# Performance work log

Hardware: AMD Instinct MI355X
Metric: run time of the kernel (lower is better)

Reference implementation:

```python
import jax, jax.numpy as jnp
import numpy as np

B, S, D, H = 2, 2048, 1024, 16
DH = D // H


def setup_inputs() -> dict:
    key = jax.random.key(0)
    ks = jax.random.split(key, 12)
    f = lambda k, sh: jax.random.normal(k, sh, dtype=jnp.float32)
    inp = {"q": f(ks[0], (B, S, D)), "k": f(ks[1], (B, S, D)), "v": f(ks[2], (B, S, D))}
    scale = 1.0 / np.sqrt(D)
    names = ["q", "k", "v", "o"]
    for i, n in enumerate(names):
        inp["W" + n] = f(ks[3 + i], (D, D)) * scale
        inp["b" + n] = f(ks[7 + i], (D,)) * scale
    # causal mask: True = masked out
    inp["mask"] = jnp.triu(jnp.ones((S, S), dtype=bool), k=1)[None, None]
    return inp


def _rope(x):
    # x: [b, h, s, dh]; non-standard RoPE from AbsPositionEncoding
    s, dh = x.shape[2], x.shape[3]
    inv = jnp.exp(jnp.arange(0, dh, 2, dtype=jnp.float32) * (-(4.0 * jnp.log(jnp.float32(10.0))) / dh))
    pos = jnp.arange(s, dtype=jnp.float32)[:, None]
    sin = jnp.sin(pos * inv)  # [s, dh/2]
    cos = jnp.cos(pos * inv)
    x1 = x[..., 0::2]
    x2 = x[..., 1::2]
    out = jnp.stack([x1 * sin - x2 * cos, -x1 * cos - x2 * sin], axis=-1)
    return out.reshape(x.shape)


def reference(q, k, v, Wq, bq, Wk, bk, Wv, bv, Wo, bo, mask):
    b, s, d = q.shape
    h, dh = H, DH

    def proj(x, W, bias):
        return (x @ W.T + bias).reshape(b, -1, h, dh).transpose(0, 2, 1, 3)

    Q = proj(q, Wq, bq)
    K = proj(k, Wk, bk)
    V = proj(v, Wv, bv)
    PQ = _rope(Q)
    PK = _rope(K)
    # NOTE: source's forward() path applies NO 1/sqrt(dh) scaling
    scores = jnp.einsum('bhqd,bhkd->bhqk', PQ, PK)
    neg = jnp.finfo(scores.dtype).min
    scores = jnp.where(mask, neg, scores)
    p = jax.nn.softmax(scores, axis=-1)
    p = jnp.where(mask, jnp.float32(0.0), p)
    out = jnp.einsum('bhqk,bhkd->bhqd', p, V)
    out = out.transpose(0, 2, 1, 3).reshape(b, s, d)
    return out @ Wo.T + bo
```

## Files before the change

### kernel.cpp

```cpp
#include <hip/hip_runtime.h>
#include <stdint.h>

#define BB 2
#define SS 2048
#define DD 1024
#define HH 16
#define DH 64
#define MM 4096

typedef __attribute__((ext_vector_type(8))) short short8;
typedef __attribute__((ext_vector_type(4))) float floatx4;
typedef __attribute__((ext_vector_type(16))) float floatx16;
typedef unsigned short u16;

#define MFMA16(a,b,c) __builtin_amdgcn_mfma_f32_16x16x32_bf16((a),(b),(c),0,0,0)
#define MFMA32(a,b,c) __builtin_amdgcn_mfma_f32_32x32x16_bf16((a),(b),(c),0,0,0)

__device__ __forceinline__ u16 f2bf(float f) {
  unsigned u = __float_as_uint(f);
  u += 0x7fffu + ((u >> 16) & 1u);
  return (u16)(u >> 16);
}

__device__ __forceinline__ unsigned cvtpk(float lo, float hi2) {
  unsigned r;
  asm("v_cvt_pk_bf16_f32 %0, %1, %2" : "=v"(r) : "v"(lo), "v"(hi2));
  return r;
}

__device__ __forceinline__ void gll16(const void* g, void* l) {
  __builtin_amdgcn_global_load_lds((const __attribute__((address_space(1))) void*)g,
                                   (__attribute__((address_space(3))) void*)l,
                                   16, 0, 0);
}

__global__ __launch_bounds__(256) void prep(
    const float* __restrict__ q, const float* __restrict__ k, const float* __restrict__ v,
    const float* __restrict__ Wq, const float* __restrict__ Wk,
    const float* __restrict__ Wv, const float* __restrict__ Wo,
    u16* __restrict__ qb, u16* __restrict__ kb, u16* __restrict__ vb,
    u16* __restrict__ wqb, u16* __restrict__ wkb, u16* __restrict__ wvb, u16* __restrict__ wob,
    float2* __restrict__ tab) {
  int bid = blockIdx.x;
  if (bid < 256) {
    const int t = bid * 256 + threadIdx.x;
    const int s = t >> 5, j = t & 31;
    const float inv = expf(-(float)j * (0.125f * 2.302585092994046f));
    const float a = (float)s * inv;
    tab[t] = make_float2(sinf(a), cosf(a));
    return;
  }
  bid -= 256;
  const float* src;
  u16* dst;
  int x;
  if (bid < 12288) {
    const int z = bid >> 12;
    x = bid & 4095;
    src = z == 0 ? q : (z == 1 ? k : v);
    dst = z == 0 ? qb : (z == 1 ? kb : vb);
  } else {
    bid -= 12288;
    const int z = bid >> 10;
    x = bid & 1023;
    src = z == 0 ? Wq : (z == 1 ? Wk : (z == 2 ? Wv : Wo));
    dst = z == 0 ? wqb : (z == 1 ? wkb : (z == 2 ? wvb : wob));
  }
  const int i = (x * 256 + threadIdx.x) * 4;
  const float4 xv = *(const float4*)(src + i);
  ushort4 p; p.x = f2bf(xv.x); p.y = f2bf(xv.y); p.z = f2bf(xv.z); p.w = f2bf(xv.w);
  *(ushort4*)(dst + i) = p;
}

__device__ __forceinline__ void gemm_core128(const u16* __restrict__ A, const u16* __restrict__ Bt,
                                             int K, u16* As, u16* Bs, floatx4 acc[4][4],
                                             int m0, int n0) {
  const int tid = threadIdx.x;
  const int w = tid >> 6, l = tid & 63;
  const int lr = l & 15, lq = l >> 4;
  const int wm = (w >> 1) * 64, wn = (w & 1) * 64;

#pragma unroll
  for (int i = 0; i < 4; ++i)
#pragma unroll
    for (int j = 0; j < 4; ++j) acc[i][j] = (floatx4){0.f, 0.f, 0.f, 0.f};

  const int srow = w * 32 + (l >> 2);
  const int scol = (l & 3) * 8;
  const u16* ag = A + (size_t)(m0 + srow) * K + scol;
  const u16* bg = Bt + (size_t)(n0 + srow) * K + scol;
  u16* as0 = &As[w * 1024];
  u16* bs0 = &Bs[w * 1024];

  for (int k0 = 0; k0 < K; k0 += 32) {
    gll16(ag + k0, as0);
    gll16(ag + (size_t)16 * K + k0, as0 + 512);
    gll16(bg + k0, bs0);
    gll16(bg + (size_t)16 * K + k0, bs0 + 512);
    __syncthreads();
    short8 af[4], bfv[4];
#pragma unroll
    for (int i = 0; i < 4; ++i) af[i] = *(const short8*)&As[(wm + i * 16 + lr) * 32 + lq * 8];
#pragma unroll
    for (int j = 0; j < 4; ++j) bfv[j] = *(const short8*)&Bs[(wn + j * 16 + lr) * 32 + lq * 8];
    __builtin_amdgcn_s_setprio(1);
#pragma unroll
    for (int i = 0; i < 4; ++i)
#pragma unroll
      for (int j = 0; j < 4; ++j) acc[i][j] = MFMA16(af[i], bfv[j], acc[i][j]);
    __builtin_amdgcn_s_setprio(0);
    __syncthreads();
  }
}

__device__ __forceinline__ void gemm_core64(const u16* __restrict__ A, const u16* __restrict__ Bt,
                                            int K, u16* As, u16* Bs, floatx4 acc[2][4],
                                            int m0, int n0) {
  const int tid = threadIdx.x;
  const int w = tid >> 6, l = tid & 63;
  const int lr = l & 15, lq = l >> 4;
  const int wm = (w >> 1) * 32, wn = (w & 1) * 64;

#pragma unroll
  for (int i = 0; i < 2; ++i)
#pragma unroll
    for (int j = 0; j < 4; ++j) acc[i][j] = (floatx4){0.f, 0.f, 0.f, 0.f};

  const int arow = w * 16 + (l >> 2);
  const int brow = w * 32 + (l >> 2);
  const int scol = (l & 3) * 8;
  const u16* ag = A + (size_t)(m0 + arow) * K + scol;
  const u16* bg = Bt + (size_t)(n0 + brow) * K + scol;
  u16* as0 = &As[w * 512];
  u16* bs0 = &Bs[w * 1024];

  for (int k0 = 0; k0 < K; k0 += 32) {
    gll16(ag + k0, as0);
    gll16(bg + k0, bs0);
    gll16(bg + (size_t)16 * K + k0, bs0 + 512);
    __syncthreads();
    short8 af[2], bfv[4];
#pragma unroll
    for (int i = 0; i < 2; ++i) af[i] = *(const short8*)&As[(wm + i * 16 + lr) * 32 + lq * 8];
#pragma unroll
    for (int j = 0; j < 4; ++j) bfv[j] = *(const short8*)&Bs[(wn + j * 16 + lr) * 32 + lq * 8];
    __builtin_amdgcn_s_setprio(1);
#pragma unroll
    for (int i = 0; i < 2; ++i)
#pragma unroll
      for (int j = 0; j < 4; ++j) acc[i][j] = MFMA16(af[i], bfv[j], acc[i][j]);
    __builtin_amdgcn_s_setprio(0);
    __syncthreads();
  }
}

__global__ __launch_bounds__(256) void gemm3_fused(
    const u16* __restrict__ A0, const u16* __restrict__ A1, const u16* __restrict__ A2,
    const u16* __restrict__ B0, const u16* __restrict__ B1, const u16* __restrict__ B2,
    const float* __restrict__ c0, const float* __restrict__ c1, const float* __restrict__ c2,
    u16* __restrict__ Qro, u16* __restrict__ Kro, u16* __restrict__ Vtr,
    const float2* __restrict__ tab) {
  __shared__ alignas(16) u16 As[128 * 32];
  __shared__ alignas(16) u16 Bs[128 * 32];
  const int z = blockIdx.z;
  const u16* A = z == 0 ? A0 : (z == 1 ? A1 : A2);
  const u16* Bt = z == 0 ? B0 : (z == 1 ? B1 : B2);
  const float* bias = z == 0 ? c0 : (z == 1 ? c1 : c2);
  const int m0 = blockIdx.y * 128, n0 = blockIdx.x * 128;

  floatx4 acc[4][4];
  gemm_core128(A, Bt, DD, As, Bs, acc, m0, n0);

  const int tid = threadIdx.x;
  const int w = tid >> 6, l = tid & 63;
  const int lr = l & 15, lq = l >> 4;
  const int wm = (w >> 1) * 64, wn = (w & 1) * 64;

  if (z == 2) {
#pragma unroll
    for (int i = 0; i < 4; ++i) {
      const int row = m0 + wm + i * 16 + lq * 4;
      const int b = row >> 11, s = row & (SS - 1);
#pragma unroll
      for (int j = 0; j < 4; ++j) {
        const int col = n0 + wn + j * 16 + lr;
        const int h = col >> 6, e = col & 63;
        const float bv = bias[col];
        ushort4 pk;
        pk.x = f2bf(acc[i][j][0] + bv);
        pk.y = f2bf(acc[i][j][1] + bv);
        pk.z = f2bf(acc[i][j][2] + bv);
        pk.w = f2bf(acc[i][j][3] + bv);
        *(ushort4*)(Vtr + ((size_t)(b * HH + h) * DH + e) * SS + s) = pk;
      }
    }
  } else {
    u16* dst = z ? Kro : Qro;
#pragma unroll
    for (int i = 0; i < 4; ++i) {
#pragma unroll
      for (int j = 0; j < 4; ++j) {
        const int col = n0 + wn + j * 16 + lr;
        const int h = col >> 6, e = col & 63;
        const float bv = bias[col];
#pragma unroll
        for (int r = 0; r < 4; ++r) {
          const int row = m0 + wm + i * 16 + lq * 4 + r;
          const int b = row >> 11, s = row & (SS - 1);
          const float v = acc[i][j][r] + bv;
          const float p = __shfl_xor(v, 1);
          const float2 sc = tab[s * 32 + (e >> 1)];
          const float ov = ((e & 1) == 0) ? (v * sc.x - p * sc.y)
                                          : (-p * sc.y - v * sc.x);
          dst[((size_t)(b * HH + h) * SS + s) * DH + e] = f2bf(ov);
        }
      }
    }
  }
}

__global__ __launch_bounds__(256) void gemm_bt(const u16* __restrict__ A, const u16* __restrict__ Bt,
                                               const float* __restrict__ bias, float* __restrict__ C,
                                               int M, int N, int K) {
  __shared__ alignas(16) u16 As[64 * 32];
  __shared__ alignas(16) u16 Bs[128 * 32];
  const int m0 = blockIdx.y * 64, n0 = blockIdx.x * 128;
  floatx4 acc[2][4];
  gemm_core64(A, Bt, K, As, Bs, acc, m0, n0);

  const int tid = threadIdx.x;
  const int w = tid >> 6, l = tid & 63;
  const int lr = l & 15, lq = l >> 4;
  const int wm = (w >> 1) * 32, wn = (w & 1) * 64;
#pragma unroll
  for (int i = 0; i < 2; ++i) {
    const int row = m0 + wm + i * 16 + lq * 4;
#pragma unroll
    for (int j = 0; j < 4; ++j) {
      const int col = n0 + wn + j * 16 + lr;
      const float bv = bias[col];
      float* cp = C + (size_t)row * N + col;
#pragma unroll
      for (int r = 0; r < 4; ++r) cp[(size_t)r * N] = acc[i][j][r] + bv;
    }
  }
}

__global__ __launch_bounds__(64) void attn_fwd(const u16* __restrict__ Qr, const u16* __restrict__ Kr,
                                               const u16* __restrict__ Vt, u16* __restrict__ O) {
  const int bid = blockIdx.x;
  const int qi = 63 - (bid >> 5);
  const int bh = bid & 31;
  const int l = threadIdx.x;
  const int ql = l & 31, hi = l >> 5;
  const int qw0 = qi * 32;
  const u16* Qh = Qr + (size_t)bh * SS * DH;
  const u16* Kh = Kr + (size_t)bh * SS * DH;
  const u16* Vh = Vt + (size_t)bh * DH * SS;

  short8 qf[4];
#pragma unroll
  for (int i = 0; i < 4; ++i)
    qf[i] = *(const short8*)(Qh + (size_t)(qw0 + ql) * DH + i * 16 + hi * 8);

  floatx16 oacc[2];
#pragma unroll
  for (int dt = 0; dt < 2; ++dt)
#pragma unroll
    for (int r = 0; r < 16; ++r) oacc[dt][r] = 0.f;
  float mrun = -1e30f, lrun = 0.f;

  const u16* kbase = Kh + (size_t)ql * DH + hi * 8;
  const u16* vbase = Vh + (size_t)ql * SS + hi * 8;

#define LOADK(kd, kv0)                                                      \
  do {                                                                      \
    const u16* kp_ = kbase + (size_t)(kv0) * DH;                            \
    kd[0] = *(const short8*)(kp_);                                          \
    kd[1] = *(const short8*)(kp_ + 16);                                     \
    kd[2] = *(const short8*)(kp_ + 32);                                     \
    kd[3] = *(const short8*)(kp_ + 48);                                     \
  } while (0)

#define COMPUTE(kd, tt)                                                              \
  do {                                                                               \
    const int kv0_ = (tt) * 32;                                                      \
    floatx16 st;                                                                     \
    _Pragma("unroll") for (int r = 0; r < 16; ++r) st[r] = 0.f;                      \
    __builtin_amdgcn_s_setprio(1);                                                   \
    _Pragma("unroll") for (int i = 0; i < 4; ++i) st = MFMA32(kd[i], qf[i], st);     \
    __builtin_amdgcn_s_setprio(0);                                                   \
    short8 vf[4];                                                                    \
    {                                                                                \
      const u16* vp_ = vbase + kv0_;                                                 \
      vf[0] = *(const short8*)(vp_);                                                 \
      vf[1] = *(const short8*)(vp_ + 16);                                            \
      vf[2] = *(const short8*)(vp_ + (size_t)32 * SS);                               \
      vf[3] = *(const short8*)(vp_ + (size_t)32 * SS + 16);                          \
    }                                                                                \
    if ((tt) == T - 1) {                             \
      _Pragma("unroll") for (int r = 0; r < 16; ++r) {                               \
        const int kv = (r & 3) + 8 * (r >> 2) + 4 * hi;                              \
        if (kv > ql) st[r] = -1e30f;                                                 \
      }                                                                              \
    }                                                                                \
    float m8[8];                                                                     \
    _Pragma("unroll") for (int r = 0; r < 8; ++r) m8[r] = fmaxf(st[r], st[r + 8]);   \
    float m4a = fmaxf(m8[0], m8[4]), m4b = fmaxf(m8[1], m8[5]);                      \
    float m4c = fmaxf(m8[2], m8[6]), m4d = fmaxf(m8[3], m8[7]);                      \
    float tmax = fmaxf(fmaxf(m4a, m4b), fmaxf(m4c, m4d));                            \
    tmax = fmaxf(tmax, __shfl_xor(tmax, 32));                                        \
    const float mn = fmaxf(mrun, tmax);                                              \
    const float sc = __expf(mrun - mn);                                              \
    mrun = mn;                                                                       \
    float ps = 0.f;                                                                  \
    _Pragma("unroll") for (int r = 0; r < 16; ++r) {                                 \
      const float p = __expf(st[r] - mn);                                            \
      st[r] = p;                                                                     \
      ps += p;                                                                       \
    }                                                                                \
    ps += __shfl_xor(ps, 32);                                                        \
    lrun = lrun * sc + ps;                                                           \
    _Pragma("unroll") for (int dt = 0; dt < 2; ++dt)                                 \
      _Pragma("unroll") for (int r = 0; r < 16; ++r) oacc[dt][r] *= sc;              \
    short8 pfrag[2];                                                                 \
    _Pragma("unroll") for (int c = 0; c < 2; ++c) {                                  \
      const int A0r = 2 * c, A1r = A0r + 1;                                          \
      const unsigned P00 = cvtpk(st[4 * A0r + 0], st[4 * A0r + 1]);                  \
      const unsigned P01 = cvtpk(st[4 * A0r + 2], st[4 * A0r + 3]);                  \
      const unsigned P10 = cvtpk(st[4 * A1r + 0], st[4 * A1r + 1]);                  \
      const unsigned P11 = cvtpk(st[4 * A1r + 2], st[4 * A1r + 3]);                  \
      const unsigned S0 = hi ? P00 : P10;                                            \
      const unsigned S1 = hi ? P01 : P11;                                            \
      const unsigned R0 = (unsigned)__shfl_xor((int)S0, 32);                         \
      const unsigned R1 = (unsigned)__shfl_xor((int)S1, 32);                         \
      union { unsigned u[4]; short8 s; } fd;                                         \
      fd.u[0] = hi ? R0 : P00;                                                       \
      fd.u[1] = hi ? R1 : P01;                                                       \
      fd.u[2] = hi ? P10 : R0;                                                       \
      fd.u[3] = hi ? P11 : R1;                                                       \
      pfrag[c] = fd.s;                                                               \
    }                                                                                \
    __builtin_amdgcn_s_setprio(1);                                                   \
    _Pragma("unroll") for (int dt = 0; dt < 2; ++dt)                                 \
      _Pragma("unroll") for (int c = 0; c < 2; ++c)                                  \
        oacc[dt] = MFMA32(vf[dt * 2 + c], pfrag[c], oacc[dt]);                       \
    __builtin_amdgcn_s_setprio(0);                                                   \
  } while (0)

  const int T = qi + 1;
  short8 kA[4], kB[4];
  LOADK(kA, 0);
  int t = 0;
  while (true) {
    if (t + 1 < T) LOADK(kB, (t + 1) * 32);
    COMPUTE(kA, t);
    ++t;
    if (t >= T) break;
    if (t + 1 < T) LOADK(kA, (t + 1) * 32);
    COMPUTE(kB, t);
    ++t;
    if (t >= T) break;
  }
#undef COMPUTE
#undef LOADK

  const float inv = 1.0f / lrun;
  const int b = bh >> 4, h = bh & 15;
  u16* orow = O + ((size_t)(b * SS + qw0 + ql)) * DD + h * DH;
#pragma unroll
  for (int dt = 0; dt < 2; ++dt)
#pragma unroll
    for (int g = 0; g < 4; ++g) {
      ushort4 pk;
      pk.x = f2bf(oacc[dt][4 * g + 0] * inv);
      pk.y = f2bf(oacc[dt][4 * g + 1] * inv);
      pk.z = f2bf(oacc[dt][4 * g + 2] * inv);
      pk.w = f2bf(oacc[dt][4 * g + 3] * inv);
      *(ushort4*)(orow + dt * 32 + 8 * g + 4 * hi) = pk;
    }
}

extern "C" void kernel_launch(void* const* d_in, const int* in_sizes, int n_in,
                              void* d_out, int out_size, void* d_ws, size_t ws_size,
                              hipStream_t stream) {
  (void)in_sizes; (void)n_in; (void)out_size; (void)ws_size;
  const float* q  = (const float*)d_in[0];
  const float* k  = (const float*)d_in[1];
  const float* v  = (const float*)d_in[2];
  const float* Wq = (const float*)d_in[3];
  const float* bq = (const float*)d_in[4];
  const float* Wk = (const float*)d_in[5];
  const float* bk = (const float*)d_in[6];
  const float* Wv = (const float*)d_in[7];
  const float* bv = (const float*)d_in[8];
  const float* Wo = (const float*)d_in[9];
  const float* bo = (const float*)d_in[10];
  float* out = (float*)d_out;

  char* ws = (char*)d_ws;
  size_t off = 0;
  auto carve = [&](size_t bytes) { char* p = ws + off; off += (bytes + 255) & ~(size_t)255; return p; };
  u16* qb   = (u16*)carve((size_t)MM * DD * 2);
  u16* kb   = (u16*)carve((size_t)MM * DD * 2);
  u16* vb   = (u16*)carve((size_t)MM * DD * 2);
  u16* wqb  = (u16*)carve((size_t)DD * DD * 2);
  u16* wkb  = (u16*)carve((size_t)DD * DD * 2);
  u16* wvb  = (u16*)carve((size_t)DD * DD * 2);
  u16* wob  = (u16*)carve((size_t)DD * DD * 2);
  u16* Qro  = (u16*)carve((size_t)MM * DD * 2);
  u16* Kro  = (u16*)carve((size_t)MM * DD * 2);
  u16* Vtr  = (u16*)carve((size_t)MM * DD * 2);
  float2* tab = (float2*)carve((size_t)SS * 32 * 8);
  u16* Ob = qb;

  prep<<<256 + 3 * 4096 + 4 * 1024, 256, 0, stream>>>(q, k, v, Wq, Wk, Wv, Wo,
                                                      qb, kb, vb, wqb, wkb, wvb, wob, tab);
  gemm3_fused<<<dim3(DD / 128, MM / 128, 3), 256, 0, stream>>>(qb, kb, vb, wqb, wkb, wvb,
                                                               bq, bk, bv, Qro, Kro, Vtr, tab);
  attn_fwd<<<64 * BB * HH, 64, 0, stream>>>(Qro, Kro, Vtr, Ob);
  gemm_bt<<<dim3(DD / 128, MM / 64), 256, 0, stream>>>(Ob, wob, bo, out, MM, DD, DD);
}
```

Measured before the change: 282.3 us.

## Split attention KV range across two waves and merge partial softmax states

Each attention block now runs two wavefronts, each covering half of the causal key tiles for the same 32-query tile. The first wave writes its running max, sum and output accumulator to shared memory, and the second wave merges them with its own state (flash-decoding style) before writing the result. This halves the serial chain of key tiles per block and doubles the number of wavefronts, which should help latency hiding and load balance for long causal rows. In exchange it adds a shared-memory merge step and a block barrier, and raises per-block LDS use.

```diff
diff --git a/kernel.cpp b/kernel.cpp
--- a/kernel.cpp
+++ b/kernel.cpp
@@ -246,12 +246,15 @@
   }
 }
 
-__global__ __launch_bounds__(64) void attn_fwd(const u16* __restrict__ Qr, const u16* __restrict__ Kr,
-                                               const u16* __restrict__ Vt, u16* __restrict__ O) {
+__global__ __launch_bounds__(128) void attn_fwd(const u16* __restrict__ Qr, const u16* __restrict__ Kr,
+                                                const u16* __restrict__ Vt, u16* __restrict__ O) {
+  __shared__ float Ms[64], Ls[64];
+  __shared__ float Os[64][33];
   const int bid = blockIdx.x;
   const int qi = 63 - (bid >> 5);
   const int bh = bid & 31;
-  const int l = threadIdx.x;
+  const int w = threadIdx.x >> 6;
+  const int l = threadIdx.x & 63;
   const int ql = l & 31, hi = l >> 5;
   const int qw0 = qi * 32;
   const u16* Qh = Qr + (size_t)bh * SS * DH;
@@ -349,36 +352,57 @@
   } while (0)
 
   const int T = qi + 1;
-  short8 kA[4], kB[4];
-  LOADK(kA, 0);
-  int t = 0;
-  while (true) {
-    if (t + 1 < T) LOADK(kB, (t + 1) * 32);
-    COMPUTE(kA, t);
-    ++t;
-    if (t >= T) break;
-    if (t + 1 < T) LOADK(kA, (t + 1) * 32);
-    COMPUTE(kB, t);
-    ++t;
-    if (t >= T) break;
+  const int Th = (T + 1) >> 1;
+  const int tbeg = w ? Th : 0;
+  const int tend = w ? T : Th;
+
+  if (tbeg < tend) {
+    short8 kA[4], kB[4];
+    LOADK(kA, tbeg * 32);
+    int t = tbeg;
+    while (true) {
+      if (t + 1 < tend) LOADK(kB, (t + 1) * 32);
+      COMPUTE(kA, t);
+      ++t;
+      if (t >= tend) break;
+      if (t + 1 < tend) LOADK(kA, (t + 1) * 32);
+      COMPUTE(kB, t);
+      ++t;
+      if (t >= tend) break;
+    }
   }
 #undef COMPUTE
 #undef LOADK
 
-  const float inv = 1.0f / lrun;
-  const int b = bh >> 4, h = bh & 15;
-  u16* orow = O + ((size_t)(b * SS + qw0 + ql)) * DD + h * DH;
-#pragma unroll
-  for (int dt = 0; dt < 2; ++dt)
-#pragma unroll
-    for (int g = 0; g < 4; ++g) {
-      ushort4 pk;
-      pk.x = f2bf(oacc[dt][4 * g + 0] * inv);
-      pk.y = f2bf(oacc[dt][4 * g + 1] * inv);
-      pk.z = f2bf(oacc[dt][4 * g + 2] * inv);
-      pk.w = f2bf(oacc[dt][4 * g + 3] * inv);
-      *(ushort4*)(orow + dt * 32 + 8 * g + 4 * hi) = pk;
-    }
+  if (w == 0) {
+    Ms[l] = mrun;
+    Ls[l] = lrun;
+#pragma unroll
+    for (int dt = 0; dt < 2; ++dt)
+#pragma unroll
+      for (int r = 0; r < 16; ++r) Os[l][dt * 16 + r] = oacc[dt][r];
+  }
+  __syncthreads();
+  if (w == 1) {
+    const float m1 = Ms[l], l1 = Ls[l];
+    const float mm = fmaxf(m1, mrun);
+    const float a1 = __expf(m1 - mm);
+    const float a2 = __expf(mrun - mm);
+    const float inv = 1.0f / (l1 * a1 + lrun * a2);
+    const int b = bh >> 4, h = bh & 15;
+    u16* orow = O + ((size_t)(b * SS + qw0 + ql)) * DD + h * DH;
+#pragma unroll
+    for (int dt = 0; dt < 2; ++dt)
+#pragma unroll
+      for (int g = 0; g < 4; ++g) {
+        ushort4 pk;
+        pk.x = f2bf((Os[l][dt * 16 + 4 * g + 0] * a1 + oacc[dt][4 * g + 0] * a2) * inv);
+        pk.y = f2bf((Os[l][dt * 16 + 4 * g + 1] * a1 + oacc[dt][4 * g + 1] * a2) * inv);
+        pk.z = f2bf((Os[l][dt * 16 + 4 * g + 2] * a1 + oacc[dt][4 * g + 2] * a2) * inv);
+        pk.w = f2bf((Os[l][dt * 16 + 4 * g + 3] * a1 + oacc[dt][4 * g + 3] * a2) * inv);
+        *(ushort4*)(orow + dt * 32 + 8 * g + 4 * hi) = pk;
+      }
+  }
 }
 
 extern "C" void kernel_launch(void* const* d_in, const int* in_sizes, int n_in,
@@ -418,6 +442,6 @@
                                                       qb, kb, vb, wqb, wkb, wvb, wob, tab);
   gemm3_fused<<<dim3(DD / 128, MM / 128, 3), 256, 0, stream>>>(qb, kb, vb, wqb, wkb, wvb,
                                                                bq, bk, bv, Qro, Kro, Vtr, tab);
-  attn_fwd<<<64 * BB * HH, 64, 0, stream>>>(Qro, Kro, Vtr, Ob);
+  attn_fwd<<<64 * BB * HH, 128, 0, stream>>>(Qro, Kro, Vtr, Ob);
   gemm_bt<<<dim3(DD / 128, MM / 64), 256, 0, stream>>>(Ob, wob, bo, out, MM, DD, DD);
 }
```

Result: faster. 271.5 us (-3.8%).
